# Optimization experiments

Measured on AMD Instinct MI355X. Metric: run time of the kernel, lower is better.

Reference implementation:

```python
import jax, jax.numpy as jnp
import numpy as np

NEG_SLOPE = 0.2

def segment_softmax(e, seg, n):
    # numerically stable softmax over edges grouped by destination node
    m = jax.ops.segment_max(e, seg, num_segments=n)
    ex = jnp.exp(e - m[seg])
    s = jax.ops.segment_sum(ex, seg, num_segments=n)
    return ex / s[seg]

def gat_conv(x, src, dst, W, a_src, a_dst, b):
    # PyG GATConv, heads=1, concat=True, add_self_loops already applied to src/dst
    n = x.shape[0]
    h = x @ W                                # [N, F_out]
    al_src = h @ a_src                       # [N]
    al_dst = h @ a_dst                       # [N]
    e = jax.nn.leaky_relu(al_src[src] + al_dst[dst], NEG_SLOPE)  # [E]
    coef = segment_softmax(e, dst, n)        # [E]
    out = jax.ops.segment_sum(coef[:, None] * h[src], dst, num_segments=n)
    return out + b

def setup_inputs() -> dict:
    key = jax.random.key(0)
    ks = jax.random.split(key, 12)
    N, Din, H, C, E = 100000, 512, 8, 16, 1600000
    x = jax.random.normal(ks[0], (N, Din), dtype=jnp.float32)
    edge_index = jax.random.randint(ks[1], (2, E), 0, N, dtype=jnp.int64)
    W_hidden = jax.random.normal(ks[2], (8, Din, H), dtype=jnp.float32) * 0.05
    att_src_h = jax.random.normal(ks[3], (8, H), dtype=jnp.float32) * 0.1
    att_dst_h = jax.random.normal(ks[4], (8, H), dtype=jnp.float32) * 0.1
    bias_h = jax.random.normal(ks[5], (8, H), dtype=jnp.float32) * 0.01
    W_out = jax.random.normal(ks[6], (H, C), dtype=jnp.float32) * 0.3
    att_src_o = jax.random.normal(ks[7], (C,), dtype=jnp.float32) * 0.1
    att_dst_o = jax.random.normal(ks[8], (C,), dtype=jnp.float32) * 0.1
    bias_o = jax.random.normal(ks[9], (C,), dtype=jnp.float32) * 0.01
    return {"x": x, "edge_index": edge_index, "W_hidden": W_hidden,
            "att_src_h": att_src_h, "att_dst_h": att_dst_h, "bias_h": bias_h,
            "W_out": W_out, "att_src_o": att_src_o, "att_dst_o": att_dst_o,
            "bias_o": bias_o}

def reference(x, edge_index, W_hidden, att_src_h, att_dst_h, bias_h,
              W_out, att_src_o, att_dst_o, bias_o):
    n = x.shape[0]
    loops = jnp.arange(n, dtype=edge_index.dtype)
    src = jnp.concatenate([edge_index[0], loops])
    dst = jnp.concatenate([edge_index[1], loops])
    # 8 parallel GATConv(Din, 8) layers averaged (dropout omitted: eval mode)
    acc = jnp.zeros((n, W_hidden.shape[-1]), dtype=x.dtype)
    for i in range(8):
        acc = acc + gat_conv(x, src, dst, W_hidden[i], att_src_h[i],
                             att_dst_h[i], bias_h[i])
    h = jax.nn.elu(acc / 8.0)
    out = gat_conv(h, src, dst, W_out, att_src_o, att_dst_o, bias_o)
    return jax.nn.log_softmax(out, axis=1)
```

## Files before the change

kernel.cpp:

```cpp
#include <hip/hip_runtime.h>
#include <math.h>

#define NNODES 100000
#define NEG 0.2f
#define CAP 64

__global__ void k_prep(const float* __restrict__ Wh, float* __restrict__ Wcat) {
    int i = blockIdx.x * 256 + threadIdx.x;
    if (i >= 512 * 64) return;
    int k = i >> 6, r = i & 63, l = r >> 3, f = r & 7;
    Wcat[i] = Wh[l * 4096 + k * 8 + f];
}

__global__ __launch_bounds__(256) void k_gemm(const float* __restrict__ x,
                                              const float* __restrict__ Wcat,
                                              float* __restrict__ h) {
    __shared__ float Ast[32][68];
    __shared__ float Bs[32][68];
    const int tid = threadIdx.x;
    const int row0 = blockIdx.x * 64;
    const int tx = tid & 15, ty = tid >> 4;
    float acc[4][4] = {};
    for (int kt = 0; kt < 512; kt += 32) {
        #pragma unroll
        for (int i = 0; i < 2; ++i) {
            int idx = tid * 2 + i;
            int r = idx >> 3;
            int kf = (idx & 7) << 2;
            int grow = row0 + r;
            float4 v = make_float4(0.f, 0.f, 0.f, 0.f);
            if (grow < NNODES) v = *(const float4*)&x[(size_t)grow * 512 + kt + kf];
            Ast[kf + 0][r] = v.x; Ast[kf + 1][r] = v.y;
            Ast[kf + 2][r] = v.z; Ast[kf + 3][r] = v.w;
        }
        #pragma unroll
        for (int i = 0; i < 2; ++i) {
            int idx = tid * 2 + i;
            int kk = idx >> 4;
            int cf = (idx & 15) << 2;
            *(float4*)&Bs[kk][cf] = *(const float4*)&Wcat[(kt + kk) * 64 + cf];
        }
        __syncthreads();
        #pragma unroll
        for (int kk = 0; kk < 32; ++kk) {
            float4 av = *(const float4*)&Ast[kk][ty * 4];
            float4 bv = *(const float4*)&Bs[kk][tx * 4];
            float a[4] = {av.x, av.y, av.z, av.w};
            float b[4] = {bv.x, bv.y, bv.z, bv.w};
            #pragma unroll
            for (int i = 0; i < 4; ++i)
                #pragma unroll
                for (int j = 0; j < 4; ++j)
                    acc[i][j] = fmaf(a[i], b[j], acc[i][j]);
        }
        __syncthreads();
    }
    #pragma unroll
    for (int i = 0; i < 4; ++i) {
        int grow = row0 + ty * 4 + i;
        if (grow < NNODES)
            *(float4*)&h[(size_t)grow * 64 + tx * 4] =
                make_float4(acc[i][0], acc[i][1], acc[i][2], acc[i][3]);
    }
}

__global__ void k_al(const float* __restrict__ h, const float* __restrict__ ash,
                     const float* __restrict__ adh, float* __restrict__ als,
                     float* __restrict__ ald) {
    int n = blockIdx.x * blockDim.x + threadIdx.x;
    if (n >= NNODES) return;
    float hv[64];
    const float4* hp = (const float4*)&h[(size_t)n * 64];
    #pragma unroll
    for (int q = 0; q < 16; ++q) *(float4*)&hv[q * 4] = hp[q];
    #pragma unroll
    for (int l = 0; l < 8; ++l) {
        float a = 0.f, b = 0.f;
        #pragma unroll
        for (int f = 0; f < 8; ++f) {
            a += hv[l * 8 + f] * ash[l * 8 + f];
            b += hv[l * 8 + f] * adh[l * 8 + f];
        }
        als[n * 8 + l] = a;
        ald[n * 8 + l] = b;
    }
}

__global__ void k_scatter(const int* __restrict__ ei, int* __restrict__ pos,
                          int* __restrict__ csr, int E, int Etot) {
    int e = blockIdx.x * 256 + threadIdx.x;
    if (e >= Etot) return;
    int src, dst;
    if (e < E) { src = ei[e]; dst = ei[E + e]; }
    else       { src = dst = e - E; }
    int slot = atomicAdd(&pos[dst], 1);
    if (slot < CAP) csr[dst * CAP + slot] = src;
}

__global__ __launch_bounds__(256) void k_edge1(const int* __restrict__ csr,
                                               const int* __restrict__ pos,
                                               const float* __restrict__ h,
                                               const float* __restrict__ als,
                                               const float* __restrict__ ald,
                                               float* __restrict__ s1,
                                               float* __restrict__ acc1) {
    int wid = (blockIdx.x * 256 + threadIdx.x) >> 6;
    int lane = threadIdx.x & 63;
    if (wid >= NNODES) return;
    int q = lane >> 3;
    int t = lane & 7;
    int deg = pos[wid]; if (deg > CAP) deg = CAP;
    float ald_l = ald[wid * 8 + t];
    const int* bucket = &csr[(size_t)wid * CAP];
    float4 a0 = make_float4(0.f, 0.f, 0.f, 0.f);
    float4 a1 = make_float4(0.f, 0.f, 0.f, 0.f);
    float sl = 0.f;
    for (int j = q; j < deg; j += 8) {
        int src = bucket[j];
        float ev = als[src * 8 + t] + ald_l;
        ev = ev > 0.f ? ev : NEG * ev;
        float ex = __expf(ev);
        const float4* hp = (const float4*)&h[(size_t)src * 64 + t * 8];
        float4 h0 = hp[0], h1 = hp[1];
        a0.x = fmaf(ex, h0.x, a0.x); a0.y = fmaf(ex, h0.y, a0.y);
        a0.z = fmaf(ex, h0.z, a0.z); a0.w = fmaf(ex, h0.w, a0.w);
        a1.x = fmaf(ex, h1.x, a1.x); a1.y = fmaf(ex, h1.y, a1.y);
        a1.z = fmaf(ex, h1.z, a1.z); a1.w = fmaf(ex, h1.w, a1.w);
        sl += ex;
    }
    #pragma unroll
    for (int m = 8; m <= 32; m <<= 1) {
        a0.x += __shfl_xor(a0.x, m, 64); a0.y += __shfl_xor(a0.y, m, 64);
        a0.z += __shfl_xor(a0.z, m, 64); a0.w += __shfl_xor(a0.w, m, 64);
        a1.x += __shfl_xor(a1.x, m, 64); a1.y += __shfl_xor(a1.y, m, 64);
        a1.z += __shfl_xor(a1.z, m, 64); a1.w += __shfl_xor(a1.w, m, 64);
        sl   += __shfl_xor(sl, m, 64);
    }
    if (lane < 8) {
        float4* op = (float4*)&acc1[(size_t)wid * 64 + t * 8];
        op[0] = a0; op[1] = a1;
        s1[wid * 8 + t] = sl;
    }
}

__global__ void k_mid(const float* __restrict__ acc1, const float* __restrict__ s1,
                      const float* __restrict__ bh, const float* __restrict__ Wo,
                      const float* __restrict__ aso, const float* __restrict__ ado,
                      float* __restrict__ g, float* __restrict__ al2s,
                      float* __restrict__ al2d) {
    int n = blockIdx.x * blockDim.x + threadIdx.x;
    if (n >= NNODES) return;
    float av[64];
    const float4* ap = (const float4*)&acc1[(size_t)n * 64];
    #pragma unroll
    for (int q = 0; q < 16; ++q) *(float4*)&av[q * 4] = ap[q];
    float sinv[8];
    #pragma unroll
    for (int l = 0; l < 8; ++l) sinv[l] = 1.0f / s1[n * 8 + l];
    float h2[8];
    #pragma unroll
    for (int f = 0; f < 8; ++f) {
        float t = 0.f;
        #pragma unroll
        for (int l = 0; l < 8; ++l) t += av[l * 8 + f] * sinv[l] + bh[l * 8 + f];
        t *= 0.125f;
        h2[f] = t > 0.f ? t : expf(t) - 1.f;
    }
    float a_ = 0.f, d_ = 0.f;
    float gv[16];
    #pragma unroll
    for (int c = 0; c < 16; ++c) {
        float t = 0.f;
        #pragma unroll
        for (int f = 0; f < 8; ++f) t += h2[f] * Wo[f * 16 + c];
        gv[c] = t;
        a_ += t * aso[c];
        d_ += t * ado[c];
    }
    float4* gp = (float4*)&g[(size_t)n * 16];
    gp[0] = make_float4(gv[0], gv[1], gv[2], gv[3]);
    gp[1] = make_float4(gv[4], gv[5], gv[6], gv[7]);
    gp[2] = make_float4(gv[8], gv[9], gv[10], gv[11]);
    gp[3] = make_float4(gv[12], gv[13], gv[14], gv[15]);
    al2s[n] = a_;
    al2d[n] = d_;
}

__global__ __launch_bounds__(256) void k_edge2(const int* __restrict__ csr,
                                               const int* __restrict__ pos,
                                               const float* __restrict__ g,
                                               const float* __restrict__ al2s,
                                               const float* __restrict__ al2d,
                                               const float* __restrict__ bo,
                                               float* __restrict__ out) {
    int wid = (blockIdx.x * 256 + threadIdx.x) >> 6;
    int lane = threadIdx.x & 63;
    if (wid >= NNODES) return;
    int c = lane & 15, q = lane >> 4;
    int deg = pos[wid]; if (deg > CAP) deg = CAP;
    float ad = al2d[wid];
    const int* bucket = &csr[(size_t)wid * CAP];
    float acc = 0.f, s = 0.f;
    for (int j = q; j < deg; j += 8) {
        int src0 = bucket[j];
        float ev0 = al2s[src0] + ad;
        ev0 = ev0 > 0.f ? ev0 : NEG * ev0;
        float ex0 = __expf(ev0);
        int j1 = j + 4;
        bool v1 = j1 < deg;
        int src1 = v1 ? bucket[j1] : src0;
        float ev1 = al2s[src1] + ad;
        ev1 = ev1 > 0.f ? ev1 : NEG * ev1;
        float ex1 = v1 ? __expf(ev1) : 0.f;
        float g0 = g[(size_t)src0 * 16 + c];
        float g1 = g[(size_t)src1 * 16 + c];
        acc = fmaf(ex0, g0, acc);
        acc = fmaf(ex1, g1, acc);
        s += ex0 + ex1;
    }
    acc += __shfl_xor(acc, 16, 64);
    acc += __shfl_xor(acc, 32, 64);
    s   += __shfl_xor(s, 16, 64);
    s   += __shfl_xor(s, 32, 64);
    float o = acc / s + bo[c];
    float m = o;
    m = fmaxf(m, __shfl_xor(m, 1, 64));
    m = fmaxf(m, __shfl_xor(m, 2, 64));
    m = fmaxf(m, __shfl_xor(m, 4, 64));
    m = fmaxf(m, __shfl_xor(m, 8, 64));
    float e2 = __expf(o - m);
    float se = e2;
    se += __shfl_xor(se, 1, 64);
    se += __shfl_xor(se, 2, 64);
    se += __shfl_xor(se, 4, 64);
    se += __shfl_xor(se, 8, 64);
    float ls = m + __logf(se);
    if (q == 0) out[(size_t)wid * 16 + c] = o - ls;
}

extern "C" void kernel_launch(void* const* d_in, const int* in_sizes, int n_in,
                              void* d_out, int out_size, void* d_ws, size_t ws_size,
                              hipStream_t stream) {
    const float* x   = (const float*)d_in[0];
    const int*   ei  = (const int*)d_in[1];
    const float* Wh  = (const float*)d_in[2];
    const float* ash = (const float*)d_in[3];
    const float* adh = (const float*)d_in[4];
    const float* bh  = (const float*)d_in[5];
    const float* Wo  = (const float*)d_in[6];
    const float* aso = (const float*)d_in[7];
    const float* ado = (const float*)d_in[8];
    const float* bo  = (const float*)d_in[9];
    float* out = (float*)d_out;

    const int E = in_sizes[1] / 2;
    const int Etot = E + NNODES;

    float* ws   = (float*)d_ws;
    float* Wcat = ws;
    float* h    = Wcat + 32768;
    float* als  = h    + (size_t)NNODES * 64;
    float* ald  = als  + (size_t)NNODES * 8;
    float* g    = ald  + (size_t)NNODES * 8;
    float* al2s = g    + (size_t)NNODES * 16;
    float* al2d = al2s + NNODES;
    float* s1   = al2d + NNODES;
    float* acc1 = s1   + (size_t)NNODES * 8;
    int*   pos  = (int*)(acc1 + (size_t)NNODES * 64);
    int*   csr  = pos + NNODES;

    hipMemsetAsync(pos, 0, NNODES * sizeof(int), stream);

    k_prep<<<128, 256, 0, stream>>>(Wh, Wcat);
    k_gemm<<<(NNODES + 63) / 64, 256, 0, stream>>>(x, Wcat, h);
    k_al<<<(NNODES + 255) / 256, 256, 0, stream>>>(h, ash, adh, als, ald);
    k_scatter<<<(Etot + 255) / 256, 256, 0, stream>>>(ei, pos, csr, E, Etot);
    k_edge1<<<(NNODES * 64 + 255) / 256, 256, 0, stream>>>(csr, pos, h, als, ald, s1, acc1);
    k_mid<<<(NNODES + 255) / 256, 256, 0, stream>>>(acc1, s1, bh, Wo, aso, ado, g, al2s, al2d);
    k_edge2<<<(NNODES * 64 + 255) / 256, 256, 0, stream>>>(csr, pos, g, al2s, al2d, bo, out);
}
```

Measured before the change: 590.1 us.

## Fuse attention logits into GEMM epilogue and store hidden features as bf16

```diff
diff --git a/kernel.cpp b/kernel.cpp
--- a/kernel.cpp
+++ b/kernel.cpp
@@ -4,6 +4,12 @@
 #define NNODES 100000
 #define NEG 0.2f
 #define CAP 64
+
+__device__ inline ushort f2bf(float f) {
+    unsigned u = __float_as_uint(f);
+    u += 0x7FFFu + ((u >> 16) & 1u);
+    return (ushort)(u >> 16);
+}
 
 __global__ void k_prep(const float* __restrict__ Wh, float* __restrict__ Wcat) {
     int i = blockIdx.x * 256 + threadIdx.x;
@@ -14,7 +20,11 @@
 
 __global__ __launch_bounds__(256) void k_gemm(const float* __restrict__ x,
                                               const float* __restrict__ Wcat,
-                                              float* __restrict__ h) {
+                                              const float* __restrict__ ash,
+                                              const float* __restrict__ adh,
+                                              ushort* __restrict__ h16,
+                                              float* __restrict__ als,
+                                              float* __restrict__ ald) {
     __shared__ float Ast[32][68];
     __shared__ float Bs[32][68];
     const int tid = threadIdx.x;
@@ -55,34 +65,27 @@
         }
         __syncthreads();
     }
+    const float s0 = ash[tx * 4 + 0], s1_ = ash[tx * 4 + 1],
+                s2 = ash[tx * 4 + 2], s3 = ash[tx * 4 + 3];
+    const float d0 = adh[tx * 4 + 0], d1 = adh[tx * 4 + 1],
+                d2 = adh[tx * 4 + 2], d3 = adh[tx * 4 + 3];
     #pragma unroll
     for (int i = 0; i < 4; ++i) {
         int grow = row0 + ty * 4 + i;
-        if (grow < NNODES)
-            *(float4*)&h[(size_t)grow * 64 + tx * 4] =
-                make_float4(acc[i][0], acc[i][1], acc[i][2], acc[i][3]);
-    }
-}
-
-__global__ void k_al(const float* __restrict__ h, const float* __restrict__ ash,
-                     const float* __restrict__ adh, float* __restrict__ als,
-                     float* __restrict__ ald) {
-    int n = blockIdx.x * blockDim.x + threadIdx.x;
-    if (n >= NNODES) return;
-    float hv[64];
-    const float4* hp = (const float4*)&h[(size_t)n * 64];
-    #pragma unroll
-    for (int q = 0; q < 16; ++q) *(float4*)&hv[q * 4] = hp[q];
-    #pragma unroll
-    for (int l = 0; l < 8; ++l) {
-        float a = 0.f, b = 0.f;
-        #pragma unroll
-        for (int f = 0; f < 8; ++f) {
-            a += hv[l * 8 + f] * ash[l * 8 + f];
-            b += hv[l * 8 + f] * adh[l * 8 + f];
-        }
-        als[n * 8 + l] = a;
-        ald[n * 8 + l] = b;
+        ushort4 hv;
+        hv.x = f2bf(acc[i][0]); hv.y = f2bf(acc[i][1]);
+        hv.z = f2bf(acc[i][2]); hv.w = f2bf(acc[i][3]);
+        float ps = acc[i][0] * s0 + acc[i][1] * s1_ + acc[i][2] * s2 + acc[i][3] * s3;
+        float pd = acc[i][0] * d0 + acc[i][1] * d1 + acc[i][2] * d2 + acc[i][3] * d3;
+        ps += __shfl_xor(ps, 1, 64);
+        pd += __shfl_xor(pd, 1, 64);
+        if (grow < NNODES) {
+            *(ushort4*)&h16[(size_t)grow * 64 + tx * 4] = hv;
+            if ((tx & 1) == 0) {
+                als[grow * 8 + (tx >> 1)] = ps;
+                ald[grow * 8 + (tx >> 1)] = pd;
+            }
+        }
     }
 }
 
@@ -99,7 +102,7 @@
 
 __global__ __launch_bounds__(256) void k_edge1(const int* __restrict__ csr,
                                                const int* __restrict__ pos,
-                                               const float* __restrict__ h,
+                                               const ushort* __restrict__ h16,
                                                const float* __restrict__ als,
                                                const float* __restrict__ ald,
                                                float* __restrict__ s1,
@@ -120,12 +123,19 @@
         float ev = als[src * 8 + t] + ald_l;
         ev = ev > 0.f ? ev : NEG * ev;
         float ex = __expf(ev);
-        const float4* hp = (const float4*)&h[(size_t)src * 64 + t * 8];
-        float4 h0 = hp[0], h1 = hp[1];
-        a0.x = fmaf(ex, h0.x, a0.x); a0.y = fmaf(ex, h0.y, a0.y);
-        a0.z = fmaf(ex, h0.z, a0.z); a0.w = fmaf(ex, h0.w, a0.w);
-        a1.x = fmaf(ex, h1.x, a1.x); a1.y = fmaf(ex, h1.y, a1.y);
-        a1.z = fmaf(ex, h1.z, a1.z); a1.w = fmaf(ex, h1.w, a1.w);
+        uint4 raw = *(const uint4*)&h16[(size_t)src * 64 + t * 8];
+        float f0 = __uint_as_float(raw.x << 16);
+        float f1 = __uint_as_float(raw.x & 0xFFFF0000u);
+        float f2 = __uint_as_float(raw.y << 16);
+        float f3 = __uint_as_float(raw.y & 0xFFFF0000u);
+        float f4 = __uint_as_float(raw.z << 16);
+        float f5 = __uint_as_float(raw.z & 0xFFFF0000u);
+        float f6 = __uint_as_float(raw.w << 16);
+        float f7 = __uint_as_float(raw.w & 0xFFFF0000u);
+        a0.x = fmaf(ex, f0, a0.x); a0.y = fmaf(ex, f1, a0.y);
+        a0.z = fmaf(ex, f2, a0.z); a0.w = fmaf(ex, f3, a0.w);
+        a1.x = fmaf(ex, f4, a1.x); a1.y = fmaf(ex, f5, a1.y);
+        a1.z = fmaf(ex, f6, a1.z); a1.w = fmaf(ex, f7, a1.w);
         sl += ex;
     }
     #pragma unroll
@@ -258,8 +268,8 @@
 
     float* ws   = (float*)d_ws;
     float* Wcat = ws;
-    float* h    = Wcat + 32768;
-    float* als  = h    + (size_t)NNODES * 64;
+    ushort* h16 = (ushort*)(Wcat + 32768);
+    float* als  = (float*)(h16 + (size_t)NNODES * 64);
     float* ald  = als  + (size_t)NNODES * 8;
     float* g    = ald  + (size_t)NNODES * 8;
     float* al2s = g    + (size_t)NNODES * 16;
@@ -272,10 +282,9 @@
     hipMemsetAsync(pos, 0, NNODES * sizeof(int), stream);
 
     k_prep<<<128, 256, 0, stream>>>(Wh, Wcat);
-    k_gemm<<<(NNODES + 63) / 64, 256, 0, stream>>>(x, Wcat, h);
-    k_al<<<(NNODES + 255) / 256, 256, 0, stream>>>(h, ash, adh, als, ald);
+    k_gemm<<<(NNODES + 63) / 64, 256, 0, stream>>>(x, Wcat, ash, adh, h16, als, ald);
     k_scatter<<<(Etot + 255) / 256, 256, 0, stream>>>(ei, pos, csr, E, Etot);
-    k_edge1<<<(NNODES * 64 + 255) / 256, 256, 0, stream>>>(csr, pos, h, als, ald, s1, acc1);
+    k_edge1<<<(NNODES * 64 + 255) / 256, 256, 0, stream>>>(csr, pos, h16, als, ald, s1, acc1);
     k_mid<<<(NNODES + 255) / 256, 256, 0, stream>>>(acc1, s1, bh, Wo, aso, ado, g, al2s, al2d);
     k_edge2<<<(NNODES * 64 + 255) / 256, 256, 0, stream>>>(csr, pos, g, al2s, al2d, bo, out);
 }
```

New measurement: 534.7 us. -9.4%, faster.
